# Optimization experiments

Hardware: AMD Instinct MI355X
Metric: run time of the kernel (lower is better)

The kernel has to match this reference:

```python
import jax, jax.numpy as jnp
import numpy as np

B, C, Q, E = 32, 1024, 64, 256  # batch, max_context_len, max_question_len, embedding_size
FE = 4 * E                      # final_encoding_size (self_attention=False)


def setup_inputs() -> dict:
    key = jax.random.key(0)
    ks = jax.random.split(key, 7)
    return {
        "context": jax.random.normal(ks[0], (B, C, E), dtype=jnp.float32),
        "question": jax.random.normal(ks[1], (B, Q, E), dtype=jnp.float32),
        "context_mask": jnp.ones((B, C), dtype=jnp.float32),
        "w_question": jax.random.normal(ks[2], (E,), dtype=jnp.float32),
        "w_context": jax.random.normal(ks[3], (E,), dtype=jnp.float32),
        "w_multiple": jax.random.normal(ks[4], (E,), dtype=jnp.float32),
        "final_W": jax.random.normal(ks[5], (FE, FE), dtype=jnp.float32) * (1.0 / np.sqrt(FE)),
        "final_b": jnp.zeros((FE,), dtype=jnp.float32),
    }


def reference(context, question, context_mask, w_question, w_context, w_multiple, final_W, final_b):
    # Trilinear similarity: s[b,c,q] = <w_q, q_q> + <w_c, c_c> + <w_m, c_c * q_q>
    q_weighted = question @ w_question                 # (B, Q)
    ctx_weighted = context @ w_context                 # (B, C)
    # (question.unsqueeze(1) * context.unsqueeze(2)) @ w_multiple, computed
    # without materializing the (B, C, Q, E) intermediate:
    mult = jnp.einsum('bce,bqe->bcq', context * w_multiple, question)  # (B, C, Q)
    similarity = ctx_weighted[:, :, None] + q_weighted[:, None, :] + mult  # (B, C, Q)

    # Context-to-query attention (softmax over question dim)
    c2q_att = jnp.einsum('bcq,bqe->bce', jax.nn.softmax(similarity, axis=2), question)

    # Query-to-context attention (softmax over context dim of row-max scores)
    q2c_weights = jax.nn.softmax(jnp.max(similarity, axis=2), axis=1)   # (B, C)
    q2c_att = jnp.einsum('bc,bce->be', q2c_weights, context)            # (B, E)

    attended = jnp.concatenate(
        [context, c2q_att, context * c2q_att, context * q2c_att[:, None, :]],
        axis=2)                                                          # (B, C, 4E)

    # MaskedLinear: affine map, output rows zeroed where context_mask == 0
    out = (attended @ final_W.T + final_b) * context_mask[:, :, None]    # (B, C, 4E)
    return out
```

## Files before the change

kernel.cpp:

```cpp
#include <hip/hip_runtime.h>

#define BB 32
#define CC 1024
#define QQ 64
#define EE 256
#define FE 1024
#define MM (BB*CC)

typedef __bf16 bf16_t;
typedef bf16_t bf16x8 __attribute__((ext_vector_type(8)));
typedef float f32x4 __attribute__((ext_vector_type(4)));
typedef unsigned short u16x8 __attribute__((ext_vector_type(8)));

__device__ __forceinline__ unsigned short f2bf(float f) {
  unsigned u = __float_as_uint(f);
  u += 0x7fffu + ((u >> 16) & 1u);
  return (unsigned short)(u >> 16);
}
__device__ __forceinline__ float bf2f(unsigned short u) {
  return __uint_as_float(((unsigned)u) << 16);
}

__device__ __forceinline__ void gload_lds16(const void* g, void* l) {
  __builtin_amdgcn_global_load_lds(
      (const __attribute__((address_space(1))) unsigned int*)g,
      (__attribute__((address_space(3))) unsigned int*)l, 16, 0, 0);
}

__global__ void k_prep(const float* __restrict__ question, const float* __restrict__ w_question,
                       float* __restrict__ qw,
                       const float* __restrict__ W, unsigned short* __restrict__ Wb) {
  int bx = blockIdx.x;
  if (bx < 512) {
    int gid = bx * 256 + threadIdx.x;
    int row = gid >> 6;
    int lane = gid & 63;
    const float4 q = *(const float4*)(question + (size_t)row * EE + lane * 4);
    const float4 wq = *(const float4*)(w_question + lane * 4);
    float d = q.x*wq.x + q.y*wq.y + q.z*wq.z + q.w*wq.w;
    d += __shfl_xor(d, 1);  d += __shfl_xor(d, 2);  d += __shfl_xor(d, 4);
    d += __shfl_xor(d, 8);  d += __shfl_xor(d, 16); d += __shfl_xor(d, 32);
    if (lane == 0) qw[row] = d;
  } else {
    int i = ((bx - 512) * 256 + threadIdx.x) * 4;
    float4 v = *(const float4*)(W + i);
    ushort4 o; o.x = f2bf(v.x); o.y = f2bf(v.y); o.z = f2bf(v.z); o.w = f2bf(v.w);
    *(ushort4*)(Wb + i) = o;
  }
}

#define DOT4(acc, A, Bv) acc += A.x*Bv.x + A.y*Bv.y + A.z*Bv.z + A.w*Bv.w

__launch_bounds__(256)
__global__ void k_simpv(const float* __restrict__ ctx, const float* __restrict__ question,
                        const float* __restrict__ qw_g, const float* __restrict__ w_context,
                        const float* __restrict__ w_multiple,
                        float* __restrict__ rowmax, unsigned short* __restrict__ att) {
  __shared__ float qbuf[QQ * 132];
  __shared__ float ck[64][36];
  __shared__ unsigned short Pl[QQ][68];
  __shared__ float cwl[64];
  __shared__ float qwl[QQ];
  const int tid = threadIdx.x;
  const int b = blockIdx.y;
  const int c0 = blockIdx.x * 64;
  const int tx = tid & 15, ty = tid >> 4;

  const float* qb = question + (size_t)b * (QQ * EE);
  if (tid < QQ) qwl[tid] = qw_g[b * QQ + tid];

  const int cr = tid >> 3, er = (tid & 7) * 4;
  const float* crow0 = ctx + ((size_t)(b * CC + c0 + cr)) * EE;
  const float* crow1 = crow0 + 32 * EE;
  unsigned short* arow0 = att + ((size_t)(b * CC + c0 + cr)) * FE;
  unsigned short* arow1 = arow0 + (size_t)32 * FE;
  float s[4][4] = {{0.f}};
  float cp0 = 0.f, cp1 = 0.f;

  for (int h = 0; h < 2; ++h) {
    if (h) __syncthreads();
    for (int idx = tid * 4; idx < QQ * 128; idx += 1024) {
      int row = idx >> 7, col = idx & 127;
      *(float4*)&qbuf[row * 132 + col] = *(const float4*)(qb + (size_t)row * EE + h * 128 + col);
    }
    for (int eo2 = 0; eo2 < 128; eo2 += 32) {
      const int eo = h * 128 + eo2;
      float4 cv0 = *(const float4*)(crow0 + eo + er);
      float4 cv1 = *(const float4*)(crow1 + eo + er);
      float4 wc = *(const float4*)(w_context + eo + er);
      float4 wm = *(const float4*)(w_multiple + eo + er);
      cp0 += cv0.x*wc.x + cv0.y*wc.y + cv0.z*wc.z + cv0.w*wc.w;
      cp1 += cv1.x*wc.x + cv1.y*wc.y + cv1.z*wc.z + cv1.w*wc.w;
      ushort4 u0, u1;
      u0.x = f2bf(cv0.x); u0.y = f2bf(cv0.y); u0.z = f2bf(cv0.z); u0.w = f2bf(cv0.w);
      u1.x = f2bf(cv1.x); u1.y = f2bf(cv1.y); u1.z = f2bf(cv1.z); u1.w = f2bf(cv1.w);
      *(ushort4*)(arow0 + eo + er) = u0;
      *(ushort4*)(arow1 + eo + er) = u1;
      __syncthreads();
      float4 m0, m1;
      m0.x = cv0.x*wm.x; m0.y = cv0.y*wm.y; m0.z = cv0.z*wm.z; m0.w = cv0.w*wm.w;
      m1.x = cv1.x*wm.x; m1.y = cv1.y*wm.y; m1.z = cv1.z*wm.z; m1.w = cv1.w*wm.w;
      *(float4*)&ck[cr][er] = m0;
      *(float4*)&ck[cr + 32][er] = m1;
      __syncthreads();
#pragma unroll
      for (int ee = 0; ee < 32; ee += 4) {
        float4 a0 = *(const float4*)&ck[ty +  0][ee];
        float4 a1 = *(const float4*)&ck[ty + 16][ee];
        float4 a2 = *(const float4*)&ck[ty + 32][ee];
        float4 a3 = *(const float4*)&ck[ty + 48][ee];
        float4 b0 = *(const float4*)&qbuf[(tx +  0) * 132 + eo2 + ee];
        float4 b1 = *(const float4*)&qbuf[(tx + 16) * 132 + eo2 + ee];
        float4 b2 = *(const float4*)&qbuf[(tx + 32) * 132 + eo2 + ee];
        float4 b3 = *(const float4*)&qbuf[(tx + 48) * 132 + eo2 + ee];
        DOT4(s[0][0], a0, b0); DOT4(s[0][1], a0, b1); DOT4(s[0][2], a0, b2); DOT4(s[0][3], a0, b3);
        DOT4(s[1][0], a1, b0); DOT4(s[1][1], a1, b1); DOT4(s[1][2], a1, b2); DOT4(s[1][3], a1, b3);
        DOT4(s[2][0], a2, b0); DOT4(s[2][1], a2, b1); DOT4(s[2][2], a2, b2); DOT4(s[2][3], a2, b3);
        DOT4(s[3][0], a3, b0); DOT4(s[3][1], a3, b1); DOT4(s[3][2], a3, b2); DOT4(s[3][3], a3, b3);
      }
    }
  }
  cp0 += __shfl_xor(cp0, 1); cp0 += __shfl_xor(cp0, 2); cp0 += __shfl_xor(cp0, 4);
  cp1 += __shfl_xor(cp1, 1); cp1 += __shfl_xor(cp1, 2); cp1 += __shfl_xor(cp1, 4);
  if ((tid & 7) == 0) { cwl[cr] = cp0; cwl[cr + 32] = cp1; }
  __syncthreads();

#pragma unroll
  for (int i = 0; i < 4; ++i) {
    int c = ty + 16 * i;
    float cw = cwl[c];
    float f[4], mx = -1e30f;
#pragma unroll
    for (int j = 0; j < 4; ++j) {
      f[j] = s[i][j] + cw + qwl[tx + 16 * j];
      mx = fmaxf(mx, f[j]);
    }
    mx = fmaxf(mx, __shfl_xor(mx, 1));
    mx = fmaxf(mx, __shfl_xor(mx, 2));
    mx = fmaxf(mx, __shfl_xor(mx, 4));
    mx = fmaxf(mx, __shfl_xor(mx, 8));
    float sum = 0.f;
#pragma unroll
    for (int j = 0; j < 4; ++j) { f[j] = expf(f[j] - mx); sum += f[j]; }
    sum += __shfl_xor(sum, 1);
    sum += __shfl_xor(sum, 2);
    sum += __shfl_xor(sum, 4);
    sum += __shfl_xor(sum, 8);
    float inv = 1.f / sum;
    if (tx == 0) rowmax[(size_t)b * CC + c0 + c] = mx;
#pragma unroll
    for (int j = 0; j < 4; ++j) Pl[tx + 16 * j][c] = f2bf(f[j] * inv);
  }
  __syncthreads();

  for (int ep = 0; ep < EE; ep += 64) {
    if (ep) __syncthreads();
    {
      int q = tid >> 2, e16 = (tid & 3) * 16;
      const float* src = qb + (size_t)q * EE + ep + e16;
      *(float4*)&qbuf[q * 68 + e16 +  0] = *(const float4*)(src);
      *(float4*)&qbuf[q * 68 + e16 +  4] = *(const float4*)(src + 4);
      *(float4*)&qbuf[q * 68 + e16 +  8] = *(const float4*)(src + 8);
      *(float4*)&qbuf[q * 68 + e16 + 12] = *(const float4*)(src + 12);
    }
    __syncthreads();
    float s2[4][4] = {{0.f}};
#pragma unroll 8
    for (int q = 0; q < QQ; ++q) {
      float a0 = bf2f(Pl[q][ty +  0]);
      float a1 = bf2f(Pl[q][ty + 16]);
      float a2 = bf2f(Pl[q][ty + 32]);
      float a3 = bf2f(Pl[q][ty + 48]);
      float4 bv = *(const float4*)&qbuf[q * 68 + tx * 4];
      s2[0][0] += a0 * bv.x; s2[0][1] += a0 * bv.y; s2[0][2] += a0 * bv.z; s2[0][3] += a0 * bv.w;
      s2[1][0] += a1 * bv.x; s2[1][1] += a1 * bv.y; s2[1][2] += a1 * bv.z; s2[1][3] += a1 * bv.w;
      s2[2][0] += a2 * bv.x; s2[2][1] += a2 * bv.y; s2[2][2] += a2 * bv.z; s2[2][3] += a2 * bv.w;
      s2[3][0] += a3 * bv.x; s2[3][1] += a3 * bv.y; s2[3][2] += a3 * bv.z; s2[3][3] += a3 * bv.w;
    }
#pragma unroll
    for (int i = 0; i < 4; ++i) {
      int c = ty + 16 * i;
      size_t row = (size_t)(b * CC + c0 + c);
      unsigned short* arow = att + row * (size_t)FE;
      ushort4 cu = *(const ushort4*)(arow + ep + tx * 4);
      float cx = bf2f(cu.x), cy = bf2f(cu.y), cz = bf2f(cu.z), cw = bf2f(cu.w);
      ushort4 o1, o2;
      o1.x = f2bf(s2[i][0]);       o1.y = f2bf(s2[i][1]);       o1.z = f2bf(s2[i][2]);       o1.w = f2bf(s2[i][3]);
      o2.x = f2bf(cx * s2[i][0]);  o2.y = f2bf(cy * s2[i][1]);  o2.z = f2bf(cz * s2[i][2]);  o2.w = f2bf(cw * s2[i][3]);
      *(ushort4*)(arow + 1 * EE + ep + tx * 4) = o1;
      *(ushort4*)(arow + 2 * EE + ep + tx * 4) = o2;
    }
  }
}

__global__ void k_q2c_part(const unsigned short* __restrict__ att, const float* __restrict__ rowmax,
                           float* __restrict__ part) {
  __shared__ float red[8];
  __shared__ float wl[128];
  const int b = blockIdx.y, ch = blockIdx.x, t = threadIdx.x;
  float4 v = *(const float4*)(rowmax + (size_t)b * CC + t * 4);
  float m = fmaxf(fmaxf(v.x, v.y), fmaxf(v.z, v.w));
  for (int off = 1; off < 64; off <<= 1) m = fmaxf(m, __shfl_xor(m, off));
  if ((t & 63) == 0) red[t >> 6] = m;
  __syncthreads();
  m = fmaxf(fmaxf(red[0], red[1]), fmaxf(red[2], red[3]));
  float s = expf(v.x - m) + expf(v.y - m) + expf(v.z - m) + expf(v.w - m);
  for (int off = 1; off < 64; off <<= 1) s += __shfl_xor(s, off);
  if ((t & 63) == 0) red[4 + (t >> 6)] = s;
  __syncthreads();
  float inv = 1.f / (red[4] + red[5] + red[6] + red[7]);
  if (t < 128) wl[t] = expf(rowmax[(size_t)b * CC + ch * 128 + t] - m) * inv;
  __syncthreads();
  const unsigned short* base = att + ((size_t)(b * CC + ch * 128)) * FE + t;
  float acc = 0.f;
#pragma unroll 4
  for (int c = 0; c < 128; ++c) acc += wl[c] * bf2f(base[(size_t)c * FE]);
  part[(b * 8 + ch) * EE + t] = acc;
}

__global__ void k_wmod(const unsigned short* __restrict__ Wb, const float* __restrict__ part,
                       unsigned short* __restrict__ att) {
  __shared__ float q2cl[EE];
  const int b = blockIdx.y;
  const int t = threadIdx.x;
  {
    float a = 0.f;
#pragma unroll
    for (int ch = 0; ch < 8; ++ch) a += part[(b * 8 + ch) * EE + t];
    q2cl[t] = a;
  }
  __syncthreads();
  const int n = blockIdx.x * 8 + (t >> 5);
  const int e = (t & 31) * 8;
  u16x8 w1 = *(const u16x8*)(Wb + (size_t)n * FE + e);
  u16x8 w4 = *(const u16x8*)(Wb + (size_t)n * FE + 768 + e);
  float4 g0 = *(const float4*)&q2cl[e];
  float4 g1 = *(const float4*)&q2cl[e + 4];
  u16x8 o;
  o[0] = f2bf(bf2f(w1[0]) + bf2f(w4[0]) * g0.x);
  o[1] = f2bf(bf2f(w1[1]) + bf2f(w4[1]) * g0.y);
  o[2] = f2bf(bf2f(w1[2]) + bf2f(w4[2]) * g0.z);
  o[3] = f2bf(bf2f(w1[3]) + bf2f(w4[3]) * g0.w);
  o[4] = f2bf(bf2f(w1[4]) + bf2f(w4[4]) * g1.x);
  o[5] = f2bf(bf2f(w1[5]) + bf2f(w4[5]) * g1.y);
  o[6] = f2bf(bf2f(w1[6]) + bf2f(w4[6]) * g1.z);
  o[7] = f2bf(bf2f(w1[7]) + bf2f(w4[7]) * g1.w);
  *(u16x8*)(att + ((size_t)(b * CC + n)) * FE + 768 + e) = o;
}

__launch_bounds__(256, 3)
__global__ void k_gemm(const unsigned short* __restrict__ A, const unsigned short* __restrict__ Bw,
                       const float* __restrict__ bias, const float* __restrict__ mask,
                       float* __restrict__ out) {
  __shared__ __align__(16) unsigned char LDSBUF[32768];
  bf16_t* As = (bf16_t*)LDSBUF;
  bf16_t* Bs = As + 128 * 64;
  float* sm = (float*)LDSBUF;
  const int tid = threadIdx.x;
  const int lane = tid & 63;
  const int wave = tid >> 6;
  const int wr = wave >> 1, wc = wave & 1;

  const int bid = blockIdx.x;
  const int wg = (bid & 7) * 256 + (bid >> 3);
  const int bcol = (wg & 7) * 128;
  const int brow = (wg >> 3) * 128;
  const int bb = brow >> 10;

  const int r = lane & 15, kg = lane >> 4;

  const int srow = tid >> 3;
  const int ssw = ((tid & 7) ^ (srow & 7)) * 8;
  const unsigned short* gA = A  + (size_t)(brow + srow) * FE + ssw;
  const unsigned short* gB = Bw + (size_t)(bcol + srow) * FE + ssw;
  const unsigned short* gW = A  + (size_t)(bb * CC + bcol + srow) * FE + 768 + ssw;
  bf16_t* dA = As + tid * 8;
  bf16_t* dB = Bs + tid * 8;

  f32x4 acc[4][4] = {};

  for (int k0 = 0; k0 < 768; k0 += 64) {
#pragma unroll
    for (int i = 0; i < 4; ++i)
      gload_lds16(gA + (size_t)(i * 32) * FE + k0, dA + i * 2048);
    if (k0 < 256) {
#pragma unroll
      for (int i = 0; i < 4; ++i)
        gload_lds16(gW + (size_t)(i * 32) * FE + k0, dB + i * 2048);
    } else {
#pragma unroll
      for (int i = 0; i < 4; ++i)
        gload_lds16(gB + (size_t)(i * 32) * FE + k0, dB + i * 2048);
    }
    __syncthreads();

    bf16x8 fa[4][2], fb[4][2];
#pragma unroll
    for (int m = 0; m < 4; ++m) {
      const int row_ = wr * 64 + m * 16 + r;
#pragma unroll
      for (int ks = 0; ks < 2; ++ks)
        fa[m][ks] = *(const bf16x8*)(As + row_ * 64 + (((ks * 4 + kg) ^ (row_ & 7)) * 8));
    }
#pragma unroll
    for (int n = 0; n < 4; ++n) {
      const int row_ = wc * 64 + n * 16 + r;
#pragma unroll
      for (int ks = 0; ks < 2; ++ks)
        fb[n][ks] = *(const bf16x8*)(Bs + row_ * 64 + (((ks * 4 + kg) ^ (row_ & 7)) * 8));
    }
#pragma unroll
    for (int ks = 0; ks < 2; ++ks)
#pragma unroll
      for (int m = 0; m < 4; ++m)
#pragma unroll
        for (int n = 0; n < 4; ++n)
          acc[m][n] = __builtin_amdgcn_mfma_f32_16x16x32_bf16(fa[m][ks], fb[n][ks], acc[m][n], 0, 0, 0);
    __syncthreads();
  }

  const int lrow = tid >> 3;
  const int co = (tid & 7) * 4;
#pragma unroll
  for (int m = 0; m < 4; ++m) {
    if (m) __syncthreads();
#pragma unroll
    for (int n = 0; n < 4; ++n)
#pragma unroll
      for (int reg = 0; reg < 4; ++reg)
        sm[(wr * 16 + kg * 4 + reg) * 133 + wc * 64 + n * 16 + r] = acc[m][n][reg];
    __syncthreads();
    const int grow = brow + (lrow >> 4) * 64 + m * 16 + (lrow & 15);
    const float mk = mask[grow];
    float* orow = out + (size_t)grow * FE + bcol;
#pragma unroll
    for (int j = 0; j < 4; ++j) {
      const int c = co + j * 32;
      float4 v = *(float4*)&sm[lrow * 133 + c];
      float4 bz = *(const float4*)(bias + bcol + c);
      float4 o; o.x = (v.x + bz.x) * mk; o.y = (v.y + bz.y) * mk;
      o.z = (v.z + bz.z) * mk; o.w = (v.w + bz.w) * mk;
      *(float4*)(orow + c) = o;
    }
  }
}

extern "C" void kernel_launch(void* const* d_in, const int* in_sizes, int n_in,
                              void* d_out, int out_size, void* d_ws, size_t ws_size,
                              hipStream_t stream) {
  const float* ctx  = (const float*)d_in[0];
  const float* ques = (const float*)d_in[1];
  const float* mask = (const float*)d_in[2];
  const float* w_q  = (const float*)d_in[3];
  const float* w_c  = (const float*)d_in[4];
  const float* w_m  = (const float*)d_in[5];
  const float* fW   = (const float*)d_in[6];
  const float* fb   = (const float*)d_in[7];
  float* out = (float*)d_out;

  char* ws = (char*)d_ws;
  float* qw     = (float*)(ws);
  float* rowmax = (float*)(ws + 8192);
  float* part   = (float*)(ws + 139264);
  unsigned short* attended = (unsigned short*)(ws + 1048576);
  unsigned short* Wb       = (unsigned short*)(ws + 68157440);

  k_prep<<<1536, 256, 0, stream>>>(ques, w_q, qw, fW, Wb);
  k_simpv<<<dim3(16, 32), 256, 0, stream>>>(ctx, ques, qw, w_c, w_m, rowmax, attended);
  k_q2c_part<<<dim3(8, 32), 256, 0, stream>>>(attended, rowmax, part);
  k_wmod<<<dim3(128, 32), 256, 0, stream>>>(Wb, part, attended);
  k_gemm<<<2048, 256, 0, stream>>>(attended, Wb, fb, mask, out);
}
```

Baseline: 151.6 us.

## Double-buffer GEMM LDS tiles to overlap global loads with MFMA

Converts the final GEMM main loop into a two-stage pipeline. It issues the global-to-LDS loads for the next K tile before computing on the current one, so load latency can hide behind the MFMA work. To hold both buffers, LDS grows to 64KB and the launch bound drops from 3 to 2 blocks per CU, which lowers occupancy. There is only one barrier per iteration, and it relies on the async global_load_lds being complete by the time that barrier is reached.

```diff
diff --git a/kernel.cpp b/kernel.cpp
--- a/kernel.cpp
+++ b/kernel.cpp
@@ -248,13 +248,13 @@
   *(u16x8*)(att + ((size_t)(b * CC + n)) * FE + 768 + e) = o;
 }
 
-__launch_bounds__(256, 3)
+__launch_bounds__(256, 2)
 __global__ void k_gemm(const unsigned short* __restrict__ A, const unsigned short* __restrict__ Bw,
                        const float* __restrict__ bias, const float* __restrict__ mask,
                        float* __restrict__ out) {
-  __shared__ __align__(16) unsigned char LDSBUF[32768];
-  bf16_t* As = (bf16_t*)LDSBUF;
-  bf16_t* Bs = As + 128 * 64;
+  __shared__ __align__(16) unsigned char LDSBUF[65536];
+  bf16_t* AsBase = (bf16_t*)LDSBUF;
+  bf16_t* BsBase = AsBase + 2 * 128 * 64;
   float* sm = (float*)LDSBUF;
   const int tid = threadIdx.x;
   const int lane = tid & 63;
@@ -274,26 +274,37 @@
   const unsigned short* gA = A  + (size_t)(brow + srow) * FE + ssw;
   const unsigned short* gB = Bw + (size_t)(bcol + srow) * FE + ssw;
   const unsigned short* gW = A  + (size_t)(bb * CC + bcol + srow) * FE + 768 + ssw;
-  bf16_t* dA = As + tid * 8;
-  bf16_t* dB = Bs + tid * 8;
 
   f32x4 acc[4][4] = {};
 
-  for (int k0 = 0; k0 < 768; k0 += 64) {
-#pragma unroll
-    for (int i = 0; i < 4; ++i)
-      gload_lds16(gA + (size_t)(i * 32) * FE + k0, dA + i * 2048);
-    if (k0 < 256) {
-#pragma unroll
-      for (int i = 0; i < 4; ++i)
-        gload_lds16(gW + (size_t)(i * 32) * FE + k0, dB + i * 2048);
-    } else {
-#pragma unroll
-      for (int i = 0; i < 4; ++i)
-        gload_lds16(gB + (size_t)(i * 32) * FE + k0, dB + i * 2048);
-    }
-    __syncthreads();
-
+#define STAGE(BUF, T) do {                                                    \
+    const int k0_ = (T) * 64;                                                 \
+    bf16_t* dA_ = AsBase + (BUF) * 8192 + tid * 8;                            \
+    bf16_t* dB_ = BsBase + (BUF) * 8192 + tid * 8;                            \
+    _Pragma("unroll")                                                         \
+    for (int i = 0; i < 4; ++i)                                               \
+      gload_lds16(gA + (size_t)(i * 32) * FE + k0_, dA_ + i * 2048);          \
+    if ((T) < 4) {                                                            \
+      _Pragma("unroll")                                                       \
+      for (int i = 0; i < 4; ++i)                                             \
+        gload_lds16(gW + (size_t)(i * 32) * FE + k0_, dB_ + i * 2048);        \
+    } else {                                                                  \
+      _Pragma("unroll")                                                       \
+      for (int i = 0; i < 4; ++i)                                             \
+        gload_lds16(gB + (size_t)(i * 32) * FE + k0_, dB_ + i * 2048);        \
+    }                                                                         \
+  } while (0)
+
+  STAGE(0, 0);
+  __syncthreads();
+
+#pragma unroll 1
+  for (int t = 0; t < 12; ++t) {
+    const int cur = t & 1;
+    if (t < 11) STAGE(cur ^ 1, t + 1);
+
+    const bf16_t* As = AsBase + cur * 8192;
+    const bf16_t* Bs = BsBase + cur * 8192;
     bf16x8 fa[4][2], fb[4][2];
 #pragma unroll
     for (int m = 0; m < 4; ++m) {
@@ -316,8 +327,10 @@
 #pragma unroll
         for (int n = 0; n < 4; ++n)
           acc[m][n] = __builtin_amdgcn_mfma_f32_16x16x32_bf16(fa[m][ks], fb[n][ks], acc[m][n], 0, 0, 0);
+
     __syncthreads();
   }
+#undef STAGE
 
   const int lrow = tid >> 3;
   const int co = (tid & 7) * 4;
```

Result: slower. 160.9 us (+6.1%).

## Remove prep kernel by folding qw dot and W conversion into consumers

Applied to the files above, without the earlier changes.

Drops the separate k_prep launch. Each k_simpv block now computes the question-weight dot products from its shared question tile. k_wmod reads fp32 final_W directly, and its batch-0 blocks convert only columns 256–767 of W to bf16 for the GEMM. This removes one kernel launch and a full pass over W. In exchange it adds redundant per-block qw work, an extra barrier, and doubles the W bytes k_wmod reads, since they are now fp32 for every batch.

```diff
diff --git a/kernel.cpp b/kernel.cpp
--- a/kernel.cpp
+++ b/kernel.cpp
@@ -27,33 +27,11 @@
       (__attribute__((address_space(3))) unsigned int*)l, 16, 0, 0);
 }
 
-__global__ void k_prep(const float* __restrict__ question, const float* __restrict__ w_question,
-                       float* __restrict__ qw,
-                       const float* __restrict__ W, unsigned short* __restrict__ Wb) {
-  int bx = blockIdx.x;
-  if (bx < 512) {
-    int gid = bx * 256 + threadIdx.x;
-    int row = gid >> 6;
-    int lane = gid & 63;
-    const float4 q = *(const float4*)(question + (size_t)row * EE + lane * 4);
-    const float4 wq = *(const float4*)(w_question + lane * 4);
-    float d = q.x*wq.x + q.y*wq.y + q.z*wq.z + q.w*wq.w;
-    d += __shfl_xor(d, 1);  d += __shfl_xor(d, 2);  d += __shfl_xor(d, 4);
-    d += __shfl_xor(d, 8);  d += __shfl_xor(d, 16); d += __shfl_xor(d, 32);
-    if (lane == 0) qw[row] = d;
-  } else {
-    int i = ((bx - 512) * 256 + threadIdx.x) * 4;
-    float4 v = *(const float4*)(W + i);
-    ushort4 o; o.x = f2bf(v.x); o.y = f2bf(v.y); o.z = f2bf(v.z); o.w = f2bf(v.w);
-    *(ushort4*)(Wb + i) = o;
-  }
-}
-
 #define DOT4(acc, A, Bv) acc += A.x*Bv.x + A.y*Bv.y + A.z*Bv.z + A.w*Bv.w
 
 __launch_bounds__(256)
 __global__ void k_simpv(const float* __restrict__ ctx, const float* __restrict__ question,
-                        const float* __restrict__ qw_g, const float* __restrict__ w_context,
+                        const float* __restrict__ w_question, const float* __restrict__ w_context,
                         const float* __restrict__ w_multiple,
                         float* __restrict__ rowmax, unsigned short* __restrict__ att) {
   __shared__ float qbuf[QQ * 132];
@@ -67,7 +45,6 @@
   const int tx = tid & 15, ty = tid >> 4;
 
   const float* qb = question + (size_t)b * (QQ * EE);
-  if (tid < QQ) qwl[tid] = qw_g[b * QQ + tid];
 
   const int cr = tid >> 3, er = (tid & 7) * 4;
   const float* crow0 = ctx + ((size_t)(b * CC + c0 + cr)) * EE;
@@ -76,12 +53,23 @@
   unsigned short* arow1 = arow0 + (size_t)32 * FE;
   float s[4][4] = {{0.f}};
   float cp0 = 0.f, cp1 = 0.f;
+  float qd = 0.f;
 
   for (int h = 0; h < 2; ++h) {
     if (h) __syncthreads();
     for (int idx = tid * 4; idx < QQ * 128; idx += 1024) {
       int row = idx >> 7, col = idx & 127;
       *(float4*)&qbuf[row * 132 + col] = *(const float4*)(qb + (size_t)row * EE + h * 128 + col);
+    }
+    __syncthreads();
+    {
+      const int qrow = tid >> 2, qc = (tid & 3) * 32;
+#pragma unroll
+      for (int j = 0; j < 32; j += 4) {
+        float4 qv = *(const float4*)&qbuf[qrow * 132 + qc + j];
+        float4 wv = *(const float4*)(w_question + h * 128 + qc + j);
+        DOT4(qd, qv, wv);
+      }
     }
     for (int eo2 = 0; eo2 < 128; eo2 += 32) {
       const int eo = h * 128 + eo2;
@@ -122,7 +110,9 @@
   }
   cp0 += __shfl_xor(cp0, 1); cp0 += __shfl_xor(cp0, 2); cp0 += __shfl_xor(cp0, 4);
   cp1 += __shfl_xor(cp1, 1); cp1 += __shfl_xor(cp1, 2); cp1 += __shfl_xor(cp1, 4);
+  qd  += __shfl_xor(qd, 1);  qd  += __shfl_xor(qd, 2);
   if ((tid & 7) == 0) { cwl[cr] = cp0; cwl[cr + 32] = cp1; }
+  if ((tid & 3) == 0) qwl[tid >> 2] = qd;
   __syncthreads();
 
 #pragma unroll
@@ -218,8 +208,8 @@
   part[(b * 8 + ch) * EE + t] = acc;
 }
 
-__global__ void k_wmod(const unsigned short* __restrict__ Wb, const float* __restrict__ part,
-                       unsigned short* __restrict__ att) {
+__global__ void k_wmod(const float* __restrict__ W, const float* __restrict__ part,
+                       unsigned short* __restrict__ att, unsigned short* __restrict__ Wb) {
   __shared__ float q2cl[EE];
   const int b = blockIdx.y;
   const int t = threadIdx.x;
@@ -232,20 +222,36 @@
   __syncthreads();
   const int n = blockIdx.x * 8 + (t >> 5);
   const int e = (t & 31) * 8;
-  u16x8 w1 = *(const u16x8*)(Wb + (size_t)n * FE + e);
-  u16x8 w4 = *(const u16x8*)(Wb + (size_t)n * FE + 768 + e);
+  const float* wrow = W + (size_t)n * FE;
+  float4 a0 = *(const float4*)(wrow + e);
+  float4 a1 = *(const float4*)(wrow + e + 4);
+  float4 c0 = *(const float4*)(wrow + 768 + e);
+  float4 c1 = *(const float4*)(wrow + 768 + e + 4);
   float4 g0 = *(const float4*)&q2cl[e];
   float4 g1 = *(const float4*)&q2cl[e + 4];
   u16x8 o;
-  o[0] = f2bf(bf2f(w1[0]) + bf2f(w4[0]) * g0.x);
-  o[1] = f2bf(bf2f(w1[1]) + bf2f(w4[1]) * g0.y);
-  o[2] = f2bf(bf2f(w1[2]) + bf2f(w4[2]) * g0.z);
-  o[3] = f2bf(bf2f(w1[3]) + bf2f(w4[3]) * g0.w);
-  o[4] = f2bf(bf2f(w1[4]) + bf2f(w4[4]) * g1.x);
-  o[5] = f2bf(bf2f(w1[5]) + bf2f(w4[5]) * g1.y);
-  o[6] = f2bf(bf2f(w1[6]) + bf2f(w4[6]) * g1.z);
-  o[7] = f2bf(bf2f(w1[7]) + bf2f(w4[7]) * g1.w);
+  o[0] = f2bf(a0.x + c0.x * g0.x);
+  o[1] = f2bf(a0.y + c0.y * g0.y);
+  o[2] = f2bf(a0.z + c0.z * g0.z);
+  o[3] = f2bf(a0.w + c0.w * g0.w);
+  o[4] = f2bf(a1.x + c1.x * g1.x);
+  o[5] = f2bf(a1.y + c1.y * g1.y);
+  o[6] = f2bf(a1.z + c1.z * g1.z);
+  o[7] = f2bf(a1.w + c1.w * g1.w);
   *(u16x8*)(att + ((size_t)(b * CC + n)) * FE + 768 + e) = o;
+
+  if (b == 0) {
+    const int rr = blockIdx.x * 8 + (t >> 5);
+    const int cc = 256 + (t & 31) * 16;
+    const float* src = W + (size_t)rr * FE + cc;
+    unsigned short* dst = Wb + (size_t)rr * FE + cc;
+#pragma unroll
+    for (int j = 0; j < 16; j += 4) {
+      float4 v = *(const float4*)(src + j);
+      ushort4 u; u.x = f2bf(v.x); u.y = f2bf(v.y); u.z = f2bf(v.z); u.w = f2bf(v.w);
+      *(ushort4*)(dst + j) = u;
+    }
+  }
 }
 
 __launch_bounds__(256, 3)
@@ -359,15 +365,13 @@
   float* out = (float*)d_out;
 
   char* ws = (char*)d_ws;
-  float* qw     = (float*)(ws);
   float* rowmax = (float*)(ws + 8192);
   float* part   = (float*)(ws + 139264);
   unsigned short* attended = (unsigned short*)(ws + 1048576);
   unsigned short* Wb       = (unsigned short*)(ws + 68157440);
 
-  k_prep<<<1536, 256, 0, stream>>>(ques, w_q, qw, fW, Wb);
-  k_simpv<<<dim3(16, 32), 256, 0, stream>>>(ctx, ques, qw, w_c, w_m, rowmax, attended);
+  k_simpv<<<dim3(16, 32), 256, 0, stream>>>(ctx, ques, w_q, w_c, w_m, rowmax, attended);
   k_q2c_part<<<dim3(8, 32), 256, 0, stream>>>(attended, rowmax, part);
-  k_wmod<<<dim3(128, 32), 256, 0, stream>>>(Wb, part, attended);
+  k_wmod<<<dim3(128, 32), 256, 0, stream>>>(fW, part, attended, Wb);
   k_gemm<<<2048, 256, 0, stream>>>(attended, Wb, fb, mask, out);
 }
```

Result: slower. 174.0 us (+14.8%).
